# Kernel tuning notes

Measured on AMD Instinct MI355X. Metric: run time of the kernel, lower is better.

The kernel has to match this reference:

```python
import jax, jax.numpy as jnp
import numpy as np

N = 100000
E = 1600000
F_IN = 64
DIM = 64
OUT = 2
BN_EPS = 1e-5


def setup_inputs() -> dict:
    key = jax.random.key(0)
    ks = jax.random.split(key, 12)
    s = lambda fan_in: 1.0 / np.sqrt(fan_in)
    inp = {
        "x": jax.random.normal(ks[0], (N, F_IN), dtype=jnp.float32),
        "edge_index": jax.random.randint(ks[1], (2, E), 0, N, dtype=jnp.int64),
        # conv1 MLP: Linear(F_IN, DIM) -> ReLU -> Linear(DIM, DIM)
        "W1a": jax.random.uniform(ks[2], (F_IN, DIM), jnp.float32, -s(F_IN), s(F_IN)),
        "b1a": jnp.zeros((DIM,), jnp.float32),
        "W1b": jax.random.uniform(ks[3], (DIM, DIM), jnp.float32, -s(DIM), s(DIM)),
        "b1b": jnp.zeros((DIM,), jnp.float32),
        "g1": jnp.ones((DIM,), jnp.float32),
        "be1": jnp.zeros((DIM,), jnp.float32),
        # conv5 MLP: Linear(DIM, DIM) -> ReLU -> Linear(DIM, 2)
        "W5a": jax.random.uniform(ks[4], (DIM, DIM), jnp.float32, -s(DIM), s(DIM)),
        "b5a": jnp.zeros((DIM,), jnp.float32),
        "W5b": jax.random.uniform(ks[5], (DIM, OUT), jnp.float32, -s(DIM), s(DIM)),
        "b5b": jnp.zeros((OUT,), jnp.float32),
        "g5": jnp.ones((OUT,), jnp.float32),
        "be5": jnp.zeros((OUT,), jnp.float32),
    }
    return inp


def _gin_agg(x, src, dst):
    # GINConv with eps=0: (1+eps)*x + sum_{j in N(i)} x_j
    agg = jax.ops.segment_sum(x[src], dst, num_segments=N)
    return x + agg


def _batchnorm(h, gamma, beta):
    mu = jnp.mean(h, axis=0)
    var = jnp.var(h, axis=0)  # biased, as torch BN uses for normalization
    return (h - mu) * jax.lax.rsqrt(var + BN_EPS) * gamma + beta


def reference(x, edge_index, W1a, b1a, W1b, b1b, g1, be1,
              W5a, b5a, W5b, b5b, g5, be5):
    src, dst = edge_index[0], edge_index[1]
    # conv1
    h = _gin_agg(x, src, dst)                      # [N, F_IN]
    h = jax.nn.relu(h @ W1a + b1a) @ W1b + b1b     # [N, DIM]
    h = jax.nn.relu(h)
    h = _batchnorm(h, g1, be1)
    # conv5
    h = _gin_agg(h, src, dst)                      # [N, DIM]
    h = jax.nn.relu(h @ W5a + b5a) @ W5b + b5b     # [N, OUT]
    h = jax.nn.relu(h)
    h = _batchnorm(h, g5, be5)
    return h
```

## Files before the change

kernel.cpp:

```cpp
#include <hip/hip_runtime.h>

#define NN 100000
#define FD 64
#define OUTF 2
#define NB 391
#define NBP 392
#define P1CH 4096
#define NTILE 6250

typedef short bf16x8 __attribute__((ext_vector_type(8), may_alias));
typedef float f32x4 __attribute__((ext_vector_type(4)));

__device__ inline ushort f2bf(float f) {
    uint u = __float_as_uint(f);
    uint r = (u + 0x7FFFu + ((u >> 16) & 1u)) >> 16;
    return (ushort)r;
}
__device__ inline float bf2f(ushort v) {
    return __uint_as_float(((uint)v) << 16);
}


__global__ void k_zero(float* __restrict__ p, int n) {
    int i = blockIdx.x * blockDim.x + threadIdx.x;
    if (i < n) p[i] = 0.f;
}

__global__ void k_copy4(const float4* __restrict__ s, float4* __restrict__ d, int n4) {
    int i = blockIdx.x * blockDim.x + threadIdx.x;
    int st = gridDim.x * blockDim.x;
    for (; i < n4; i += st) d[i] = s[i];
}

__global__ void k_cvt(const float4* __restrict__ x4, ushort4* __restrict__ xb4, int n4) {
    int i = blockIdx.x * blockDim.x + threadIdx.x;
    int st = gridDim.x * blockDim.x;
    for (; i < n4; i += st) {
        float4 v = x4[i];
        ushort4 w;
        w.x = f2bf(v.x);
        w.y = f2bf(v.y);
        w.z = f2bf(v.z);
        w.w = f2bf(v.w);
        xb4[i] = w;
    }
}


__global__ __launch_bounds__(256) void k_p1a2(const int* __restrict__ ei,
                                              int* __restrict__ ghist, int E_) {
    __shared__ int h[NB];
    int tid = threadIdx.x;
    for (int i = tid; i < NB; i += 256) h[i] = 0;
    __syncthreads();
    int c0 = blockIdx.x * P1CH;
    int c1 = min(c0 + P1CH, E_);
    for (int i = c0 + tid; i < c1; i += 256) {
        int d = ei[E_ + i];
        int b = min(max(d >> 8, 0), NB - 1);
        atomicAdd(&h[b], 1);
    }
    __syncthreads();
    int* row = ghist + (size_t)blockIdx.x * NBP;
    for (int i = tid; i < NB; i += 256) row[i] = h[i];
}

__global__ __launch_bounds__(512) void k_scanCol(int* __restrict__ ghist,
                                                 int* __restrict__ tot, int np1) {
    __shared__ int ts[512];
    int b = blockIdx.x;
    int tid = threadIdx.x;
    int v = (tid < np1) ? ghist[(size_t)tid * NBP + b] : 0;
    ts[tid] = v;
    __syncthreads();
    for (int off = 1; off < 512; off <<= 1) {
        int u = (tid >= off) ? ts[tid - off] : 0;
        __syncthreads();
        ts[tid] += u;
        __syncthreads();
    }
    if (tid < np1) ghist[(size_t)tid * NBP + b] = ts[tid] - v;
    if (tid == 511) tot[b] = ts[511];
}

__global__ __launch_bounds__(512) void k_scanB2(const int* __restrict__ tot,
                                                int* __restrict__ bbase,
                                                float* __restrict__ S) {
    __shared__ int ts[512];
    int tid = threadIdx.x;
    if (tid < 192) S[tid] = 0.f;
    int v = (tid < NB) ? tot[tid] : 0;
    ts[tid] = v;
    __syncthreads();
    for (int off = 1; off < 512; off <<= 1) {
        int u = (tid >= off) ? ts[tid - off] : 0;
        __syncthreads();
        ts[tid] += u;
        __syncthreads();
    }
    if (tid < NB) bbase[tid] = ts[tid] - v;
    if (tid == 511) bbase[NB] = ts[511];
}

__global__ __launch_bounds__(256) void k_p1b2(const int* __restrict__ ei,
                                              const int* __restrict__ ghist,
                                              const int* __restrict__ bbase,
                                              int* __restrict__ part, int E_) {
    __shared__ int cur[NB];
    int tid = threadIdx.x;
    const int* row = ghist + (size_t)blockIdx.x * NBP;
    for (int i = tid; i < NB; i += 256) cur[i] = bbase[i] + row[i];
    __syncthreads();
    int c0 = blockIdx.x * P1CH;
    int c1 = min(c0 + P1CH, E_);
    for (int i = c0 + tid; i < c1; i += 256) {
        int s = ei[i];
        int d = ei[E_ + i];
        int b = min(max(d >> 8, 0), NB - 1);
        int slot = atomicAdd(&cur[b], 1);
        part[slot] = ((d & 255) << 20) | (s & 0xFFFFF);
    }
}

__global__ __launch_bounds__(256) void k_build(const int* __restrict__ part,
                                               const int* __restrict__ bbase,
                                               int* __restrict__ rowptr,
                                               int* __restrict__ csr, int E_) {
    __shared__ int cnt[256];
    __shared__ int ts[256];
    __shared__ int cur[256];
    int b = blockIdx.x;
    int tid = threadIdx.x;
    cnt[tid] = 0;
    __syncthreads();
    int s0 = bbase[b], s1 = bbase[b + 1];
    for (int i = s0 + tid; i < s1; i += 256) {
        int v = part[i];
        atomicAdd(&cnt[(v >> 20) & 255], 1);
    }
    __syncthreads();
    int v = cnt[tid];
    ts[tid] = v;
    __syncthreads();
    for (int off = 1; off < 256; off <<= 1) {
        int u = (tid >= off) ? ts[tid - off] : 0;
        __syncthreads();
        ts[tid] += u;
        __syncthreads();
    }
    int excl = ts[tid] - v;
    int node = b * 256 + tid;
    if (node < NN) rowptr[node] = s0 + excl;
    cur[tid] = s0 + excl;
    if (b == 0 && tid == 0) rowptr[NN] = E_;
    __syncthreads();
    for (int i = s0 + tid; i < s1; i += 256) {
        int v2 = part[i];
        int lj = (v2 >> 20) & 255;
        int pos = atomicAdd(&cur[lj], 1);
        csr[pos] = v2 & 0xFFFFF;
    }
}


#define GSTEP(T, A0, A1, A2, A3)                                               \
    {                                                                          \
        int j = (T) * 4 + g;                                                   \
        int s = __shfl(id, j);                                                 \
        float m = (j < cnt) ? 1.f : 0.f;                                       \
        uint2 v = *(const uint2*)(Xb + (long)s * FD + (l << 2));               \
        A0 = fmaf(m, __uint_as_float(v.x << 16), A0);                          \
        A1 = fmaf(m, __uint_as_float(v.x & 0xFFFF0000u), A1);                  \
        A2 = fmaf(m, __uint_as_float(v.y << 16), A2);                          \
        A3 = fmaf(m, __uint_as_float(v.y & 0xFFFF0000u), A3);                  \
    }

__global__ __launch_bounds__(256) void k_gather2(
        const ushort* __restrict__ Xb, const int* __restrict__ rowptr,
        const int* __restrict__ csr,
        const float* __restrict__ bs, const float* __restrict__ bq,
        const float* __restrict__ gam, const float* __restrict__ bet,
        ushort* __restrict__ outb, int E_, int affine) {
    int tid = threadIdx.x;
    int lane = tid & 63;
    int n = (blockIdx.x * blockDim.x + tid) >> 6;
    if (n >= NN) return;
    int g = lane >> 4;
    int l = lane & 15;
    int start = rowptr[n], end = rowptr[n + 1];
    start = min(max(start, 0), E_);
    end = min(max(end, start), E_);
    int deg = end - start;

    float a0 = 0.f, a1 = 0.f, a2 = 0.f, a3 = 0.f;
    float b0 = 0.f, b1 = 0.f, b2 = 0.f, b3 = 0.f;
    if (g == 0) {
        uint2 v = *(const uint2*)(Xb + (long)n * FD + (l << 2));
        a0 = __uint_as_float(v.x << 16);
        a1 = __uint_as_float(v.x & 0xFFFF0000u);
        a2 = __uint_as_float(v.y << 16);
        a3 = __uint_as_float(v.y & 0xFFFF0000u);
    }

    for (int base = start; base < end; base += 64) {
        int cnt = min(end - base, 64);
        int id = 0;
        if (lane < cnt) id = min(max(csr[base + lane], 0), NN - 1);
        int nsteps = (cnt + 3) >> 2;
        int t = 0;
        for (; t + 4 <= nsteps; t += 4) {
            GSTEP(t + 0, a0, a1, a2, a3)
            GSTEP(t + 1, b0, b1, b2, b3)
            GSTEP(t + 2, a0, a1, a2, a3)
            GSTEP(t + 3, b0, b1, b2, b3)
        }
        for (; t + 2 <= nsteps; t += 2) {
            GSTEP(t + 0, a0, a1, a2, a3)
            GSTEP(t + 1, b0, b1, b2, b3)
        }
        if (t < nsteps) GSTEP(t, a0, a1, a2, a3)
    }
    a0 += b0; a1 += b1; a2 += b2; a3 += b3;
    a0 += __shfl_xor(a0, 16); a0 += __shfl_xor(a0, 32);
    a1 += __shfl_xor(a1, 16); a1 += __shfl_xor(a1, 32);
    a2 += __shfl_xor(a2, 16); a2 += __shfl_xor(a2, 32);
    a3 += __shfl_xor(a3, 16); a3 += __shfl_xor(a3, 32);

    if (g == 0) {
        if (affine) {
            float dp1 = (float)(deg + 1);
            float A[4] = {a0, a1, a2, a3};
#pragma unroll
            for (int c = 0; c < 4; c++) {
                int ch = l * 4 + c;
                float mu = bs[ch] * (1.f / NN);
                float var = bq[ch] * (1.f / NN) - mu * mu;
                float s = gam[ch] * rsqrtf(var + 1e-5f);
                float sh = fmaf(-mu, s, bet[ch]);
                A[c] = fmaf(A[c], s, dp1 * sh);
            }
            a0 = A[0]; a1 = A[1]; a2 = A[2]; a3 = A[3];
        }
        ushort4 v;
        v.x = f2bf(a0); v.y = f2bf(a1); v.z = f2bf(a2); v.w = f2bf(a3);
        ((ushort4*)(outb + (long)n * FD))[l] = v;
    }
}


__global__ __launch_bounds__(256) void k_mlp1_mfma(
        const ushort* __restrict__ Ab,
        const float* __restrict__ Wa, const float* __restrict__ ba,
        const float* __restrict__ Wb, const float* __restrict__ bb,
        ushort* __restrict__ H, float* __restrict__ gsum, float* __restrict__ gsq) {
    __shared__ __attribute__((aligned(16))) short tile[4][16 * 72];
    __shared__ float sArr[64], qArr[64];
    int tid = threadIdx.x;
    int w = tid >> 6, lane = tid & 63;
    int l = lane & 15, quad = lane >> 4;
    if (tid < 64) { sArr[tid] = 0.f; qArr[tid] = 0.f; }
    __syncthreads();

    bf16x8 B1[2][4], B2[2][4];
#pragma unroll
    for (int ks = 0; ks < 2; ks++)
#pragma unroll
        for (int t = 0; t < 4; t++) {
            bf16x8 f1, f2;
#pragma unroll
            for (int j = 0; j < 8; j++) {
                int k = ks * 32 + quad * 8 + j;
                f1[j] = (short)f2bf(Wa[k * 64 + t * 16 + l]);
                f2[j] = (short)f2bf(Wb[k * 64 + t * 16 + l]);
            }
            B1[ks][t] = f1;
            B2[ks][t] = f2;
        }
    float bias1[4], bias2[4];
#pragma unroll
    for (int t = 0; t < 4; t++) {
        bias1[t] = ba[t * 16 + l];
        bias2[t] = bb[t * 16 + l];
    }

    float s[4] = {0.f, 0.f, 0.f, 0.f}, q[4] = {0.f, 0.f, 0.f, 0.f};
    short* tp = &tile[w][0];
    int gw = blockIdx.x * 4 + w;
    int nw = gridDim.x * 4;
    for (int tau = gw; tau < NTILE; tau += nw) {
        int m0 = tau * 16;
        bf16x8 A0 = *(const bf16x8*)(Ab + (size_t)(m0 + l) * FD + quad * 8);
        bf16x8 A1 = *(const bf16x8*)(Ab + (size_t)(m0 + l) * FD + 32 + quad * 8);
#pragma unroll
        for (int t = 0; t < 4; t++) {
            f32x4 c = {0.f, 0.f, 0.f, 0.f};
            c = __builtin_amdgcn_mfma_f32_16x16x32_bf16(A0, B1[0][t], c, 0, 0, 0);
            c = __builtin_amdgcn_mfma_f32_16x16x32_bf16(A1, B1[1][t], c, 0, 0, 0);
#pragma unroll
            for (int r = 0; r < 4; r++) {
                float v = fmaxf(c[r] + bias1[t], 0.f);
                tp[(quad * 4 + r) * 72 + t * 16 + l] = (short)f2bf(v);
            }
        }
        bf16x8 A20 = *(const bf16x8*)&tp[l * 72 + quad * 8];
        bf16x8 A21 = *(const bf16x8*)&tp[l * 72 + 32 + quad * 8];
#pragma unroll
        for (int t = 0; t < 4; t++) {
            f32x4 c = {0.f, 0.f, 0.f, 0.f};
            c = __builtin_amdgcn_mfma_f32_16x16x32_bf16(A20, B2[0][t], c, 0, 0, 0);
            c = __builtin_amdgcn_mfma_f32_16x16x32_bf16(A21, B2[1][t], c, 0, 0, 0);
#pragma unroll
            for (int r = 0; r < 4; r++) {
                float v = fmaxf(c[r] + bias2[t], 0.f);
                s[t] += v;
                q[t] += v * v;
                tp[(quad * 4 + r) * 72 + t * 16 + l] = (short)f2bf(v);
            }
        }
        int row = lane >> 2, ch = lane & 3;
        bf16x8 o0 = *(const bf16x8*)&tp[row * 72 + ch * 16];
        bf16x8 o1 = *(const bf16x8*)&tp[row * 72 + ch * 16 + 8];
        *(bf16x8*)(H + (size_t)(m0 + row) * FD + ch * 16) = o0;
        *(bf16x8*)(H + (size_t)(m0 + row) * FD + ch * 16 + 8) = o1;
    }
#pragma unroll
    for (int t = 0; t < 4; t++) {
        s[t] += __shfl_xor(s[t], 16); s[t] += __shfl_xor(s[t], 32);
        q[t] += __shfl_xor(q[t], 16); q[t] += __shfl_xor(q[t], 32);
    }
    if (quad == 0) {
#pragma unroll
        for (int t = 0; t < 4; t++) {
            atomicAdd(&sArr[t * 16 + l], s[t]);
            atomicAdd(&qArr[t * 16 + l], q[t]);
        }
    }
    __syncthreads();
    if (tid < 64) {
        atomicAdd(&gsum[tid], sArr[tid]);
        atomicAdd(&gsq[tid], qArr[tid]);
    }
}

__global__ __launch_bounds__(256) void k_mlp2_mfma(
        const ushort* __restrict__ Ab,
        const float* __restrict__ Wa, const float* __restrict__ ba,
        const float* __restrict__ Wb2, const float* __restrict__ bb2,
        float* __restrict__ O, float* __restrict__ gsum, float* __restrict__ gsq) {
    __shared__ __attribute__((aligned(16))) short tile[4][16 * 72];
    __shared__ float sArr[2], qArr[2];
    int tid = threadIdx.x;
    int w = tid >> 6, lane = tid & 63;
    int l = lane & 15, quad = lane >> 4;
    if (tid < 2) { sArr[tid] = 0.f; qArr[tid] = 0.f; }
    __syncthreads();

    bf16x8 B1[2][4], B2[2];
#pragma unroll
    for (int ks = 0; ks < 2; ks++) {
#pragma unroll
        for (int t = 0; t < 4; t++) {
            bf16x8 f1;
#pragma unroll
            for (int j = 0; j < 8; j++) {
                int k = ks * 32 + quad * 8 + j;
                f1[j] = (short)f2bf(Wa[k * 64 + t * 16 + l]);
            }
            B1[ks][t] = f1;
        }
        bf16x8 f2;
#pragma unroll
        for (int j = 0; j < 8; j++) {
            int k = ks * 32 + quad * 8 + j;
            f2[j] = (l < OUTF) ? (short)f2bf(Wb2[k * OUTF + l]) : (short)0;
        }
        B2[ks] = f2;
    }
    float bias1[4];
#pragma unroll
    for (int t = 0; t < 4; t++) bias1[t] = ba[t * 16 + l];
    float bias2 = (l < OUTF) ? bb2[l] : 0.f;

    float s = 0.f, q = 0.f;
    short* tp = &tile[w][0];
    int gw = blockIdx.x * 4 + w;
    int nw = gridDim.x * 4;
    for (int tau = gw; tau < NTILE; tau += nw) {
        int m0 = tau * 16;
        bf16x8 A0 = *(const bf16x8*)(Ab + (size_t)(m0 + l) * FD + quad * 8);
        bf16x8 A1 = *(const bf16x8*)(Ab + (size_t)(m0 + l) * FD + 32 + quad * 8);
#pragma unroll
        for (int t = 0; t < 4; t++) {
            f32x4 c = {0.f, 0.f, 0.f, 0.f};
            c = __builtin_amdgcn_mfma_f32_16x16x32_bf16(A0, B1[0][t], c, 0, 0, 0);
            c = __builtin_amdgcn_mfma_f32_16x16x32_bf16(A1, B1[1][t], c, 0, 0, 0);
#pragma unroll
            for (int r = 0; r < 4; r++) {
                float v = fmaxf(c[r] + bias1[t], 0.f);
                tp[(quad * 4 + r) * 72 + t * 16 + l] = (short)f2bf(v);
            }
        }
        bf16x8 A20 = *(const bf16x8*)&tp[l * 72 + quad * 8];
        bf16x8 A21 = *(const bf16x8*)&tp[l * 72 + 32 + quad * 8];
        f32x4 c = {0.f, 0.f, 0.f, 0.f};
        c = __builtin_amdgcn_mfma_f32_16x16x32_bf16(A20, B2[0], c, 0, 0, 0);
        c = __builtin_amdgcn_mfma_f32_16x16x32_bf16(A21, B2[1], c, 0, 0, 0);
#pragma unroll
        for (int r = 0; r < 4; r++) {
            float v = fmaxf(c[r] + bias2, 0.f);
            if (l < OUTF) {
                s += v;
                q += v * v;
                O[(size_t)(m0 + quad * 4 + r) * OUTF + l] = v;
            }
        }
    }
    s += __shfl_xor(s, 16); s += __shfl_xor(s, 32);
    q += __shfl_xor(q, 16); q += __shfl_xor(q, 32);
    if (quad == 0 && l < OUTF) {
        atomicAdd(&sArr[l], s);
        atomicAdd(&qArr[l], q);
    }
    __syncthreads();
    if (tid < OUTF) {
        atomicAdd(&gsum[tid], sArr[tid]);
        atomicAdd(&gsq[tid], qArr[tid]);
    }
}

template <bool BF16OUT>
__global__ __launch_bounds__(256) void k_mlp64(
        const float* __restrict__ X,
        const float* __restrict__ Wa, const float* __restrict__ ba,
        const float* __restrict__ Wb, const float* __restrict__ bb,
        void* __restrict__ Hv, float* __restrict__ gsum, float* __restrict__ gsq) {
    __shared__ float row[256 * 65];
    int tid = threadIdx.x;
    long node = (long)blockIdx.x * 256 + tid;
    bool valid = node < NN;
    if (valid) {
        const float4* rp = (const float4*)(X + node * FD);
#pragma unroll
        for (int q = 0; q < 16; q++) {
            float4 v = rp[q];
            row[tid * 65 + 4 * q + 0] = v.x;
            row[tid * 65 + 4 * q + 1] = v.y;
            row[tid * 65 + 4 * q + 2] = v.z;
            row[tid * 65 + 4 * q + 3] = v.w;
        }
    }
    float acc[64];
#pragma unroll
    for (int j = 0; j < 64; j++) acc[j] = ba[j];
    if (valid) {
        for (int k = 0; k < 64; k++) {
            float xv = row[tid * 65 + k];
            const float* wr = Wa + k * 64;
#pragma unroll
            for (int j = 0; j < 64; j++) acc[j] = fmaf(xv, wr[j], acc[j]);
        }
    }
#pragma unroll
    for (int j = 0; j < 64; j++) row[tid * 65 + j] = fmaxf(acc[j], 0.f);
#pragma unroll
    for (int j = 0; j < 64; j++) acc[j] = bb[j];
    if (valid) {
        for (int k = 0; k < 64; k++) {
            float xv = row[tid * 65 + k];
            const float* wr = Wb + k * 64;
#pragma unroll
            for (int j = 0; j < 64; j++) acc[j] = fmaf(xv, wr[j], acc[j]);
        }
    }
#pragma unroll
    for (int j = 0; j < 64; j++) {
        float v = valid ? fmaxf(acc[j], 0.f) : 0.f;
        row[tid * 65 + j] = v;
    }
    if (valid) {
        if (BF16OUT) {
            ushort4* op = (ushort4*)((ushort*)Hv + node * FD);
#pragma unroll
            for (int q = 0; q < 16; q++) {
                ushort4 w;
                w.x = f2bf(row[tid * 65 + 4 * q + 0]);
                w.y = f2bf(row[tid * 65 + 4 * q + 1]);
                w.z = f2bf(row[tid * 65 + 4 * q + 2]);
                w.w = f2bf(row[tid * 65 + 4 * q + 3]);
                op[q] = w;
            }
        } else {
            float4* op = (float4*)((float*)Hv + node * FD);
#pragma unroll
            for (int q = 0; q < 16; q++) {
                float4 v;
                v.x = row[tid * 65 + 4 * q + 0];
                v.y = row[tid * 65 + 4 * q + 1];
                v.z = row[tid * 65 + 4 * q + 2];
                v.w = row[tid * 65 + 4 * q + 3];
                op[q] = v;
            }
        }
    }
    __syncthreads();
    if (tid < 64) {
        float s = 0.f, q = 0.f;
        for (int r = 0; r < 256; r++) {
            float v = row[r * 65 + tid];
            s += v;
            q += v * v;
        }
        atomicAdd(&gsum[tid], s);
        atomicAdd(&gsq[tid], q);
    }
}

__global__ __launch_bounds__(256) void k_mlp_out(
        const float* __restrict__ X,
        const float* __restrict__ Wa, const float* __restrict__ ba,
        const float* __restrict__ Wb, const float* __restrict__ bb,
        float* __restrict__ O, float* __restrict__ gsum, float* __restrict__ gsq) {
    __shared__ float row[256 * 65];
    __shared__ float red[256][4];
    int tid = threadIdx.x;
    long node = (long)blockIdx.x * 256 + tid;
    bool valid = node < NN;
    if (valid) {
        const float4* rp = (const float4*)(X + node * FD);
#pragma unroll
        for (int q = 0; q < 16; q++) {
            float4 v = rp[q];
            row[tid * 65 + 4 * q + 0] = v.x;
            row[tid * 65 + 4 * q + 1] = v.y;
            row[tid * 65 + 4 * q + 2] = v.z;
            row[tid * 65 + 4 * q + 3] = v.w;
        }
    }
    float acc[64];
#pragma unroll
    for (int j = 0; j < 64; j++) acc[j] = ba[j];
    if (valid) {
        for (int k = 0; k < 64; k++) {
            float xv = row[tid * 65 + k];
            const float* wr = Wa + k * 64;
#pragma unroll
            for (int j = 0; j < 64; j++) acc[j] = fmaf(xv, wr[j], acc[j]);
        }
    }
#pragma unroll
    for (int j = 0; j < 64; j++) row[tid * 65 + j] = fmaxf(acc[j], 0.f);
    float a0 = bb[0];
    float a1 = bb[1];
    if (valid) {
        for (int k = 0; k < 64; k++) {
            float xv = row[tid * 65 + k];
            a0 = fmaf(xv, Wb[k * 2 + 0], a0);
            a1 = fmaf(xv, Wb[k * 2 + 1], a1);
        }
    }
    float v0 = valid ? fmaxf(a0, 0.f) : 0.f;
    float v1 = valid ? fmaxf(a1, 0.f) : 0.f;
    if (valid) {
        float2 v;
        v.x = v0;
        v.y = v1;
        ((float2*)O)[node] = v;
    }
    red[tid][0] = v0;
    red[tid][1] = v0 * v0;
    red[tid][2] = v1;
    red[tid][3] = v1 * v1;
    __syncthreads();
    for (int off = 128; off > 0; off >>= 1) {
        if (tid < off) {
#pragma unroll
            for (int c = 0; c < 4; c++) red[tid][c] += red[tid + off][c];
        }
        __syncthreads();
    }
    if (tid == 0) {
        atomicAdd(&gsum[0], red[0][0]);
        atomicAdd(&gsq[0], red[0][1]);
        atomicAdd(&gsum[1], red[0][2]);
        atomicAdd(&gsq[1], red[0][3]);
    }
}


__global__ void k_bnfin(const float* __restrict__ gsum, const float* __restrict__ gsq,
                        const float* __restrict__ g, const float* __restrict__ be,
                        float* __restrict__ sc, float* __restrict__ sh, int C, float invN) {
    int c = threadIdx.x;
    if (c < C) {
        float mu = gsum[c] * invN;
        float var = gsq[c] * invN - mu * mu;
        float s = g[c] * rsqrtf(var + 1e-5f);
        sc[c] = s;
        sh[c] = fmaf(-mu, s, be[c]);
    }
}

__global__ void k_bn_apply2(float* __restrict__ o, const float* __restrict__ sc,
                            const float* __restrict__ sh, int n) {
    int i = blockIdx.x * blockDim.x + threadIdx.x;
    if (i < n) {
        int c = i & 1;
        o[i] = fmaf(o[i], sc[c], sh[c]);
    }
}


__global__ void k_scatter(const float* __restrict__ x, const int* __restrict__ ei,
                          float* __restrict__ agg, int E_) {
    int lane = threadIdx.x & 63;
    int wid = (blockIdx.x * blockDim.x + threadIdx.x) >> 6;
    int nw = (gridDim.x * blockDim.x) >> 6;
    for (long e = wid; e < E_; e += nw) {
        int s = ei[e];
        int d = ei[E_ + e];
        float v = x[(long)s * FD + lane];
        atomicAdd(&agg[(long)d * FD + lane], v);
    }
}

__global__ void k_scatter_bn(const float* __restrict__ h, const int* __restrict__ ei,
                             const float* __restrict__ sc, const float* __restrict__ sh,
                             float* __restrict__ agg, int E_) {
    int lane = threadIdx.x & 63;
    float scl = sc[lane];
    float shf = sh[lane];
    int wid = (blockIdx.x * blockDim.x + threadIdx.x) >> 6;
    int nw = (gridDim.x * blockDim.x) >> 6;
    for (long e = wid; e < E_; e += nw) {
        int s = ei[e];
        int d = ei[E_ + e];
        float v = fmaf(h[(long)s * FD + lane], scl, shf);
        atomicAdd(&agg[(long)d * FD + lane], v);
    }
}

__global__ void k_bn_copy(const float4* __restrict__ h, const float4* __restrict__ sc4,
                          const float4* __restrict__ sh4, float4* __restrict__ o, int n4) {
    int i = blockIdx.x * blockDim.x + threadIdx.x;
    int st = gridDim.x * blockDim.x;
    for (; i < n4; i += st) {
        float4 v = h[i];
        int c = i & 15;
        float4 s = sc4[c];
        float4 b = sh4[c];
        v.x = fmaf(v.x, s.x, b.x);
        v.y = fmaf(v.y, s.y, b.y);
        v.z = fmaf(v.z, s.z, b.z);
        v.w = fmaf(v.w, s.w, b.w);
        o[i] = v;
    }
}


extern "C" void kernel_launch(void* const* d_in, const int* in_sizes, int n_in,
                              void* d_out, int out_size, void* d_ws, size_t ws_size,
                              hipStream_t stream) {
    const float* x   = (const float*)d_in[0];
    const int*   ei  = (const int*)d_in[1];
    const float* W1a = (const float*)d_in[2];
    const float* b1a = (const float*)d_in[3];
    const float* W1b = (const float*)d_in[4];
    const float* b1b = (const float*)d_in[5];
    const float* g1  = (const float*)d_in[6];
    const float* be1 = (const float*)d_in[7];
    const float* W5a = (const float*)d_in[8];
    const float* b5a = (const float*)d_in[9];
    const float* W5b = (const float*)d_in[10];
    const float* b5b = (const float*)d_in[11];
    const float* g5  = (const float*)d_in[12];
    const float* be5 = (const float*)d_in[13];
    float* out = (float*)d_out;

    const int E = in_sizes[1] / 2;

    float* ws = (float*)d_ws;
    float* agg = ws;
    ushort* aggb = (ushort*)ws;
    ushort* xb  = (ushort*)(ws + 6400000);
    ushort* h1b = (ushort*)(ws + 9600000);
    float* h1_fb = ws + 6400000;
    float* S   = ws + 12800000;
    float* gsum1  = S;
    float* gsq1   = S + 64;
    float* gsum2  = S + 128;
    float* gsq2   = S + 160;
    float* scale1 = S + 192;
    float* shift1 = S + 256;
    float* scale2 = S + 320;
    float* shift2 = S + 328;

    int* ibase  = (int*)(S + 512);
    int* rowptr = ibase;
    int* csr    = ibase + 100004;
    int* bbase  = ibase + 100004 + E;
    int* tot    = bbase + 400;
    int* ghist  = tot + 392;
    int* part   = (int*)agg;

    const int np1 = (E + P1CH - 1) / P1CH;
    size_t needed = (size_t)(12800000 + 512) * 4 +
                    (size_t)(100004 + E + 400 + 392 + (size_t)np1 * NBP) * 4;

    const int n4 = NN * FD / 4;
    const int nblk = (NN + 255) / 256;

    if (ws_size >= needed && np1 <= 512) {
        k_cvt<<<2048, 256, 0, stream>>>((const float4*)x, (ushort4*)xb, n4);
        k_p1a2<<<np1, 256, 0, stream>>>(ei, ghist, E);
        k_scanCol<<<NB, 512, 0, stream>>>(ghist, tot, np1);
        k_scanB2<<<1, 512, 0, stream>>>(tot, bbase, S);
        k_p1b2<<<np1, 256, 0, stream>>>(ei, ghist, bbase, part, E);
        k_build<<<NB, 256, 0, stream>>>(part, bbase, rowptr, csr, E);

        k_gather2<<<25000, 256, 0, stream>>>(xb, rowptr, csr, nullptr, nullptr,
                                             nullptr, nullptr, aggb, E, 0);
        k_mlp1_mfma<<<782, 256, 0, stream>>>(aggb, W1a, b1a, W1b, b1b, h1b, gsum1, gsq1);
        k_gather2<<<25000, 256, 0, stream>>>(h1b, rowptr, csr, gsum1, gsq1,
                                             g1, be1, aggb, E, 1);
        k_mlp2_mfma<<<782, 256, 0, stream>>>(aggb, W5a, b5a, W5b, b5b, out, gsum2, gsq2);
        k_bnfin<<<1, 64, 0, stream>>>(gsum2, gsq2, g5, be5, scale2, shift2, OUTF, 1.f / NN);
        k_bn_apply2<<<(NN * OUTF + 255) / 256, 256, 0, stream>>>(out, scale2, shift2, NN * OUTF);
    } else {
        k_zero<<<1, 256, 0, stream>>>(S, 192);
        k_copy4<<<4096, 256, 0, stream>>>((const float4*)x, (float4*)agg, n4);
        k_scatter<<<4096, 256, 0, stream>>>(x, ei, agg, E);
        k_mlp64<false><<<nblk, 256, 0, stream>>>(agg, W1a, b1a, W1b, b1b,
                                                 (void*)h1_fb, gsum1, gsq1);
        k_bnfin<<<1, 64, 0, stream>>>(gsum1, gsq1, g1, be1, scale1, shift1, 64, 1.f / NN);
        k_bn_copy<<<4096, 256, 0, stream>>>((const float4*)h1_fb, (const float4*)scale1,
                                            (const float4*)shift1, (float4*)agg, n4);
        k_scatter_bn<<<4096, 256, 0, stream>>>(h1_fb, ei, scale1, shift1, agg, E);
        k_mlp_out<<<nblk, 256, 0, stream>>>(agg, W5a, b5a, W5b, b5b, out, gsum2, gsq2);
        k_bnfin<<<1, 64, 0, stream>>>(gsum2, gsq2, g5, be5, scale2, shift2, OUTF, 1.f / NN);
        k_bn_apply2<<<(NN * OUTF + 255) / 256, 256, 0, stream>>>(out, scale2, shift2, NN * OUTF);
    }
}
```

Measured before the change: 271.9 us.

## Use zero sentinel row in gather, prefetch MLP tiles, fuse final BN kernels

The gather kernel drops per-edge masking: inactive lanes now point to a zeroed sentinel row at index NN, written by the convert kernel into padded buffers, and accumulation uses packed float2 adds. Both MFMA MLP kernels software-prefetch the next tile's A operands while the current tile is computed. The final BN statistics kernel and the apply kernel are fused into one, removing a launch. The sentinel needs extra workspace padding and shifts the buffer offsets, and the prefetch adds register pressure.

```diff
diff --git a/kernel.cpp b/kernel.cpp
--- a/kernel.cpp
+++ b/kernel.cpp
@@ -10,6 +10,7 @@
 
 typedef short bf16x8 __attribute__((ext_vector_type(8), may_alias));
 typedef float f32x4 __attribute__((ext_vector_type(4)));
+typedef float f32x2 __attribute__((ext_vector_type(2)));
 
 __device__ inline ushort f2bf(float f) {
     uint u = __float_as_uint(f);
@@ -32,8 +33,14 @@
     for (; i < n4; i += st) d[i] = s[i];
 }
 
-__global__ void k_cvt(const float4* __restrict__ x4, ushort4* __restrict__ xb4, int n4) {
+__global__ void k_cvt(const float4* __restrict__ x4, ushort4* __restrict__ xb4,
+                      ushort* __restrict__ xb, ushort* __restrict__ h1b, int n4) {
     int i = blockIdx.x * blockDim.x + threadIdx.x;
+    if (i < 16) {
+        ushort4 z = {0, 0, 0, 0};
+        ((ushort4*)(xb + (size_t)NN * FD))[i] = z;
+        ((ushort4*)(h1b + (size_t)NN * FD))[i] = z;
+    }
     int st = gridDim.x * blockDim.x;
     for (; i < n4; i += st) {
         float4 v = x4[i];
@@ -163,16 +170,17 @@
 }
 
 
-#define GSTEP(T, A0, A1, A2, A3)                                               \
+#define GSTEP(T, A01, A23)                                                     \
     {                                                                          \
-        int j = (T) * 4 + g;                                                   \
-        int s = __shfl(id, j);                                                 \
-        float m = (j < cnt) ? 1.f : 0.f;                                       \
-        uint2 v = *(const uint2*)(Xb + (long)s * FD + (l << 2));               \
-        A0 = fmaf(m, __uint_as_float(v.x << 16), A0);                          \
-        A1 = fmaf(m, __uint_as_float(v.x & 0xFFFF0000u), A1);                  \
-        A2 = fmaf(m, __uint_as_float(v.y << 16), A2);                          \
-        A3 = fmaf(m, __uint_as_float(v.y & 0xFFFF0000u), A3);                  \
+        int s = __shfl(id, (T) * 4 + g);                                       \
+        uint2 v = *(const uint2*)(Xb + ((long)s << 6) + (l << 2));             \
+        f32x2 p, q2;                                                           \
+        p[0] = __uint_as_float(v.x << 16);                                     \
+        p[1] = __uint_as_float(v.x & 0xFFFF0000u);                             \
+        q2[0] = __uint_as_float(v.y << 16);                                    \
+        q2[1] = __uint_as_float(v.y & 0xFFFF0000u);                            \
+        A01 += p;                                                              \
+        A23 += q2;                                                             \
     }
 
 __global__ __launch_bounds__(256) void k_gather2(
@@ -192,44 +200,48 @@
     end = min(max(end, start), E_);
     int deg = end - start;
 
-    float a0 = 0.f, a1 = 0.f, a2 = 0.f, a3 = 0.f;
-    float b0 = 0.f, b1 = 0.f, b2 = 0.f, b3 = 0.f;
+    f32x2 a01 = {0.f, 0.f}, a23 = {0.f, 0.f};
+    f32x2 b01 = {0.f, 0.f}, b23 = {0.f, 0.f};
     if (g == 0) {
-        uint2 v = *(const uint2*)(Xb + (long)n * FD + (l << 2));
-        a0 = __uint_as_float(v.x << 16);
-        a1 = __uint_as_float(v.x & 0xFFFF0000u);
-        a2 = __uint_as_float(v.y << 16);
-        a3 = __uint_as_float(v.y & 0xFFFF0000u);
+        uint2 v = *(const uint2*)(Xb + ((long)n << 6) + (l << 2));
+        a01[0] = __uint_as_float(v.x << 16);
+        a01[1] = __uint_as_float(v.x & 0xFFFF0000u);
+        a23[0] = __uint_as_float(v.y << 16);
+        a23[1] = __uint_as_float(v.y & 0xFFFF0000u);
     }
 
     for (int base = start; base < end; base += 64) {
         int cnt = min(end - base, 64);
-        int id = 0;
+        int id = NN;
         if (lane < cnt) id = min(max(csr[base + lane], 0), NN - 1);
         int nsteps = (cnt + 3) >> 2;
         int t = 0;
         for (; t + 4 <= nsteps; t += 4) {
-            GSTEP(t + 0, a0, a1, a2, a3)
-            GSTEP(t + 1, b0, b1, b2, b3)
-            GSTEP(t + 2, a0, a1, a2, a3)
-            GSTEP(t + 3, b0, b1, b2, b3)
+            GSTEP(t + 0, a01, a23)
+            GSTEP(t + 1, b01, b23)
+            GSTEP(t + 2, a01, a23)
+            GSTEP(t + 3, b01, b23)
         }
         for (; t + 2 <= nsteps; t += 2) {
-            GSTEP(t + 0, a0, a1, a2, a3)
-            GSTEP(t + 1, b0, b1, b2, b3)
-        }
-        if (t < nsteps) GSTEP(t, a0, a1, a2, a3)
-    }
-    a0 += b0; a1 += b1; a2 += b2; a3 += b3;
-    a0 += __shfl_xor(a0, 16); a0 += __shfl_xor(a0, 32);
-    a1 += __shfl_xor(a1, 16); a1 += __shfl_xor(a1, 32);
-    a2 += __shfl_xor(a2, 16); a2 += __shfl_xor(a2, 32);
-    a3 += __shfl_xor(a3, 16); a3 += __shfl_xor(a3, 32);
+            GSTEP(t + 0, a01, a23)
+            GSTEP(t + 1, b01, b23)
+        }
+        if (t < nsteps) GSTEP(t, a01, a23)
+    }
+    a01 += b01;
+    a23 += b23;
+    float A[4] = {a01[0], a01[1], a23[0], a23[1]};
+#pragma unroll
+    for (int c = 0; c < 4; c++) {
+        float v = A[c];
+        v += __shfl_xor(v, 16);
+        v += __shfl_xor(v, 32);
+        A[c] = v;
+    }
 
     if (g == 0) {
         if (affine) {
             float dp1 = (float)(deg + 1);
-            float A[4] = {a0, a1, a2, a3};
 #pragma unroll
             for (int c = 0; c < 4; c++) {
                 int ch = l * 4 + c;
@@ -239,11 +251,10 @@
                 float sh = fmaf(-mu, s, bet[ch]);
                 A[c] = fmaf(A[c], s, dp1 * sh);
             }
-            a0 = A[0]; a1 = A[1]; a2 = A[2]; a3 = A[3];
         }
         ushort4 v;
-        v.x = f2bf(a0); v.y = f2bf(a1); v.z = f2bf(a2); v.w = f2bf(a3);
-        ((ushort4*)(outb + (long)n * FD))[l] = v;
+        v.x = f2bf(A[0]); v.y = f2bf(A[1]); v.z = f2bf(A[2]); v.w = f2bf(A[3]);
+        ((ushort4*)(outb + ((long)n << 6)))[l] = v;
     }
 }
 
@@ -287,10 +298,21 @@
     short* tp = &tile[w][0];
     int gw = blockIdx.x * 4 + w;
     int nw = gridDim.x * 4;
+    bf16x8 A0, A1;
+    if (gw < NTILE) {
+        int m0 = gw * 16;
+        A0 = *(const bf16x8*)(Ab + (size_t)(m0 + l) * FD + quad * 8);
+        A1 = *(const bf16x8*)(Ab + (size_t)(m0 + l) * FD + 32 + quad * 8);
+    }
     for (int tau = gw; tau < NTILE; tau += nw) {
         int m0 = tau * 16;
-        bf16x8 A0 = *(const bf16x8*)(Ab + (size_t)(m0 + l) * FD + quad * 8);
-        bf16x8 A1 = *(const bf16x8*)(Ab + (size_t)(m0 + l) * FD + 32 + quad * 8);
+        int nxt = tau + nw;
+        bf16x8 nA0, nA1;
+        if (nxt < NTILE) {
+            int nm0 = nxt * 16;
+            nA0 = *(const bf16x8*)(Ab + (size_t)(nm0 + l) * FD + quad * 8);
+            nA1 = *(const bf16x8*)(Ab + (size_t)(nm0 + l) * FD + 32 + quad * 8);
+        }
 #pragma unroll
         for (int t = 0; t < 4; t++) {
             f32x4 c = {0.f, 0.f, 0.f, 0.f};
@@ -322,6 +344,8 @@
         bf16x8 o1 = *(const bf16x8*)&tp[row * 72 + ch * 16 + 8];
         *(bf16x8*)(H + (size_t)(m0 + row) * FD + ch * 16) = o0;
         *(bf16x8*)(H + (size_t)(m0 + row) * FD + ch * 16 + 8) = o1;
+        A0 = nA0;
+        A1 = nA1;
     }
 #pragma unroll
     for (int t = 0; t < 4; t++) {
@@ -385,10 +409,21 @@
     short* tp = &tile[w][0];
     int gw = blockIdx.x * 4 + w;
     int nw = gridDim.x * 4;
+    bf16x8 A0, A1;
+    if (gw < NTILE) {
+        int m0 = gw * 16;
+        A0 = *(const bf16x8*)(Ab + (size_t)(m0 + l) * FD + quad * 8);
+        A1 = *(const bf16x8*)(Ab + (size_t)(m0 + l) * FD + 32 + quad * 8);
+    }
     for (int tau = gw; tau < NTILE; tau += nw) {
         int m0 = tau * 16;
-        bf16x8 A0 = *(const bf16x8*)(Ab + (size_t)(m0 + l) * FD + quad * 8);
-        bf16x8 A1 = *(const bf16x8*)(Ab + (size_t)(m0 + l) * FD + 32 + quad * 8);
+        int nxt = tau + nw;
+        bf16x8 nA0, nA1;
+        if (nxt < NTILE) {
+            int nm0 = nxt * 16;
+            nA0 = *(const bf16x8*)(Ab + (size_t)(nm0 + l) * FD + quad * 8);
+            nA1 = *(const bf16x8*)(Ab + (size_t)(nm0 + l) * FD + 32 + quad * 8);
+        }
 #pragma unroll
         for (int t = 0; t < 4; t++) {
             f32x4 c = {0.f, 0.f, 0.f, 0.f};
@@ -414,6 +449,8 @@
                 O[(size_t)(m0 + quad * 4 + r) * OUTF + l] = v;
             }
         }
+        A0 = nA0;
+        A1 = nA1;
     }
     s += __shfl_xor(s, 16); s += __shfl_xor(s, 32);
     q += __shfl_xor(q, 16); q += __shfl_xor(q, 32);
@@ -597,6 +634,22 @@
         float s = g[c] * rsqrtf(var + 1e-5f);
         sc[c] = s;
         sh[c] = fmaf(-mu, s, be[c]);
+    }
+}
+
+__global__ void k_bnfin_apply2(const float* __restrict__ gsum,
+                               const float* __restrict__ gsq,
+                               const float* __restrict__ g,
+                               const float* __restrict__ be,
+                               float* __restrict__ o, int n) {
+    int i = blockIdx.x * blockDim.x + threadIdx.x;
+    if (i < n) {
+        int c = i & 1;
+        float mu = gsum[c] * (1.f / NN);
+        float var = gsq[c] * (1.f / NN) - mu * mu;
+        float s = g[c] * rsqrtf(var + 1e-5f);
+        float sh = fmaf(-mu, s, be[c]);
+        o[i] = fmaf(o[i], s, sh);
     }
 }
 
@@ -682,9 +735,9 @@
     float* agg = ws;
     ushort* aggb = (ushort*)ws;
     ushort* xb  = (ushort*)(ws + 6400000);
-    ushort* h1b = (ushort*)(ws + 9600000);
+    ushort* h1b = (ushort*)(ws + 9600032);
     float* h1_fb = ws + 6400000;
-    float* S   = ws + 12800000;
+    float* S   = ws + 12800064;
     float* gsum1  = S;
     float* gsq1   = S + 64;
     float* gsum2  = S + 128;
@@ -703,14 +756,14 @@
     int* part   = (int*)agg;
 
     const int np1 = (E + P1CH - 1) / P1CH;
-    size_t needed = (size_t)(12800000 + 512) * 4 +
+    size_t needed = (size_t)(12800064 + 512) * 4 +
                     (size_t)(100004 + E + 400 + 392 + (size_t)np1 * NBP) * 4;
 
     const int n4 = NN * FD / 4;
     const int nblk = (NN + 255) / 256;
 
     if (ws_size >= needed && np1 <= 512) {
-        k_cvt<<<2048, 256, 0, stream>>>((const float4*)x, (ushort4*)xb, n4);
+        k_cvt<<<2048, 256, 0, stream>>>((const float4*)x, (ushort4*)xb, xb, h1b, n4);
         k_p1a2<<<np1, 256, 0, stream>>>(ei, ghist, E);
         k_scanCol<<<NB, 512, 0, stream>>>(ghist, tot, np1);
         k_scanB2<<<1, 512, 0, stream>>>(tot, bbase, S);
@@ -723,8 +776,8 @@
         k_gather2<<<25000, 256, 0, stream>>>(h1b, rowptr, csr, gsum1, gsq1,
                                              g1, be1, aggb, E, 1);
         k_mlp2_mfma<<<782, 256, 0, stream>>>(aggb, W5a, b5a, W5b, b5b, out, gsum2, gsq2);
-        k_bnfin<<<1, 64, 0, stream>>>(gsum2, gsq2, g5, be5, scale2, shift2, OUTF, 1.f / NN);
-        k_bn_apply2<<<(NN * OUTF + 255) / 256, 256, 0, stream>>>(out, scale2, shift2, NN * OUTF);
+        k_bnfin_apply2<<<(NN * OUTF + 255) / 256, 256, 0, stream>>>(gsum2, gsq2, g5, be5,
+                                                                    out, NN * OUTF);
     } else {
         k_zero<<<1, 256, 0, stream>>>(S, 192);
         k_copy4<<<4096, 256, 0, stream>>>((const float4*)x, (float4*)agg, n4);
```

Result: no change. 272.5 us (+0.2%).
